# Optimization experiments

Measured on AMD Instinct MI355X. Metric: run time of the kernel, lower is better.

## Reference

```python
import jax, jax.numpy as jnp
import numpy as np

N_HEADS = 8
HEAD_DIM = 64  # d_model // n_heads = 512 // 8


def setup_inputs() -> dict:
    key = jax.random.key(0)
    kq, kk, kv, km = jax.random.split(key, 4)
    B, C, H, L, D = 8, 4, N_HEADS, 512, HEAD_DIM
    q = jax.random.normal(kq, (B * C, H, L, D), dtype=jnp.float32)
    k = jax.random.normal(kk, (B * C, H, D, L), dtype=jnp.float32)  # pre-transposed, matmul(q, k) directly
    v = jax.random.normal(kv, (B * C, H, L, D), dtype=jnp.float32)
    attn_mask = jax.random.randint(km, (B, L, L), 0, 2).astype(bool)  # True = masked out
    return {"q": q, "k": k, "v": v, "attn_mask": attn_mask}


def reference(q, k, v, attn_mask):
    # q: [B*C, H, L, D]; k: [B*C, H, D, L]; v: [B*C, H, L, D]; attn_mask: [B, L, L] bool
    scale = jnp.asarray(HEAD_DIM ** (-0.5), dtype=q.dtype)
    scores = jnp.einsum('ghld,ghdm->ghlm', q, k) * scale  # [B*C, H, L, L]
    if attn_mask is not None:
        B = attn_mask.shape[0]
        C = q.shape[0] // B
        H, L = scores.shape[1], scores.shape[2]
        scores = scores.reshape(B, C, H, L, L)
        mask = attn_mask[:, None, None, :, :]  # broadcast over channels and heads
        scores = jnp.where(mask, -jnp.inf, scores)
        scores = scores.reshape(B * C, H, L, L)
    attn_weights = jax.nn.softmax(scores, axis=-1)  # dropout p=0.0 -> identity (eval)
    output = jnp.einsum('ghlm,ghmd->ghld', attn_weights, v)  # [B*C, H, L, D]
    return output
```

## Files before the change

### kernel.cpp

```cpp
#include <hip/hip_runtime.h>


typedef __attribute__((ext_vector_type(8)))  short bf16x8;
typedef __attribute__((ext_vector_type(16))) float f32x16;

union Frag4 { uint4 x; unsigned u[4]; bf16x8 v; };

__device__ __forceinline__ unsigned pk_bf16(float a, float b){
    unsigned ua = __builtin_bit_cast(unsigned, a) + 0x8000u;
    unsigned ub = __builtin_bit_cast(unsigned, b) + 0x8000u;
    return __builtin_amdgcn_perm(ub, ua, 0x07060302u);
}

__device__ __forceinline__ float fast_exp2(float x){
#if __has_builtin(__builtin_amdgcn_exp2f)
    return __builtin_amdgcn_exp2f(x);
#else
    return exp2f(x);
#endif
}

#define L2E 1.44269504088896f

__global__ __launch_bounds__(256)
void pack_mask(const int* __restrict__ mg, unsigned long long* __restrict__ bits)
{
    const int t    = blockIdx.x*256 + threadIdx.x;
    const int lane = t & 63;
    const int w0   = t >> 6;
    const int strd = (int)((gridDim.x*256) >> 6);
    const int nW   = 8*512*8;
    for (int i = w0; i < nW; i += strd){
        int v = mg[(size_t)i*64 + lane];
        unsigned long long m = __ballot(v != 0);
        if (lane == 0) bits[i] = m;
    }
}

__device__ __forceinline__ unsigned build_mword(const int* p, int h){
    unsigned w = 0;
    #pragma unroll
    for (int rg=0; rg<4; ++rg){
        int4 mm = *(const int4*)(p + rg*8 + h*4);
        const unsigned base = rg*8 + h*4;
        w |= (mm.x?1u:0u) << base;
        w |= (mm.y?1u:0u) << (base+1);
        w |= (mm.z?1u:0u) << (base+2);
        w |= (mm.w?1u:0u) << (base+3);
    }
    return w;
}

template<int BITS>
__global__ __launch_bounds__(128, 4)
void attn_fused(const float* __restrict__ qg, const float* __restrict__ kg,
                const float* __restrict__ vg, const int* __restrict__ mg,
                const unsigned* __restrict__ bits, float* __restrict__ og)
{
    __shared__ uint4 sKt4[64*8];
    __shared__ uint4 sVt4[64*8];

    const int t    = threadIdx.x;
    const int lane = t & 63;
    const int wv   = t >> 6;
    const int col  = lane & 31;
    const int h    = lane >> 5;

    const int bi   = blockIdx.x;
    const int s    = bi >> 3;
    const int head = (bi & 7)*32 + (s >> 3);
    const int qt   = s & 7;
    const int b    = bi & 7;

    const float* qh = qg + (size_t)head*32768;
    const float* kh = kg + (size_t)head*32768;
    const float* vh = vg + (size_t)head*32768;
    float*       oh = og + (size_t)head*32768;

    const int qrl  = wv*32 + col;
    const int qrow = qt*64 + qrl;
    const int* mrow0 = BITS ? nullptr
        : mg + (size_t)b*262144 + (size_t)qrow*512;
    const unsigned* brow = BITS
        ? bits + ((size_t)b*512 + qrow)*16
        : nullptr;

    Frag4 qf[4];
    {
        const float* qr = qh + (size_t)qrow*64 + h*8;
        #pragma unroll
        for (int kt=0; kt<4; ++kt){
            float4 x0 = *(const float4*)(qr + kt*16);
            float4 x1 = *(const float4*)(qr + kt*16 + 4);
            qf[kt].u[0] = pk_bf16(x0.x*0.125f, x0.y*0.125f);
            qf[kt].u[1] = pk_bf16(x0.z*0.125f, x0.w*0.125f);
            qf[kt].u[2] = pk_bf16(x1.x*0.125f, x1.y*0.125f);
            qf[kt].u[3] = pk_bf16(x1.z*0.125f, x1.w*0.125f);
        }
    }

    f32x16 o0, o1;
    #pragma unroll
    for (int i=0;i<16;++i){ o0[i]=0.f; o1[i]=0.f; }
    float lsum = 0.f;

    for (int kb=0; kb<8; ++kb){
        __syncthreads();

        uint2 mbv;
        if constexpr (BITS) mbv = *(const uint2*)(brow + kb*2);

        #pragma unroll
        for (int gi=0; gi<4; ++gi){
            const int g = wv*4 + gi;
            const float* kp = kh + (size_t)(g*8)*512 + kb*64 + lane;
            float kv[8];
            #pragma unroll
            for (int dd=0; dd<8; ++dd) kv[dd] = kp[(size_t)dd*512];
            Frag4 w;
            w.u[0]=pk_bf16(kv[0],kv[1]); w.u[1]=pk_bf16(kv[2],kv[3]);
            w.u[2]=pk_bf16(kv[4],kv[5]); w.u[3]=pk_bf16(kv[6],kv[7]);
            sKt4[lane*8 + (g ^ (lane&7))] = w.x;
        }
        #pragma unroll
        for (int gi=0; gi<4; ++gi){
            const int g = wv*4 + gi;
            const float* vp = vh + (size_t)(kb*64 + g*8)*64 + lane;
            float vv[8];
            #pragma unroll
            for (int mm=0; mm<8; ++mm) vv[mm] = vp[(size_t)mm*64];
            Frag4 w;
            w.u[0]=pk_bf16(vv[0],vv[1]); w.u[1]=pk_bf16(vv[2],vv[3]);
            w.u[2]=pk_bf16(vv[4],vv[5]); w.u[3]=pk_bf16(vv[6],vv[7]);
            sVt4[lane*8 + (g ^ (lane&7))] = w.x;
        }
        __syncthreads();

        const int* mrow = BITS ? nullptr : (mrow0 + kb*64);
        #pragma unroll
        for (int mt=0; mt<2; ++mt){
            f32x16 sc;
            #pragma unroll
            for (int i=0;i<16;++i) sc[i]=0.f;
            #pragma unroll
            for (int kt=0; kt<4; ++kt){
                const int r = mt*32 + col;
                Frag4 a; a.x = sKt4[r*8 + ((kt*2+h) ^ (r&7))];
                sc = __builtin_amdgcn_mfma_f32_32x32x16_bf16(a.v, qf[kt].v, sc, 0, 0, 0);
            }
            unsigned pp[8];
            if constexpr (BITS){
                const unsigned mword = mt ? mbv.y : mbv.x;
                #pragma unroll
                for (int rg=0; rg<4; ++rg){
                    const unsigned mw = mword >> (rg*8 + h*4);
                    float e0 = (mw & 1u) ? 0.f : fast_exp2(sc[4*rg+0]*L2E);
                    float e1 = (mw & 2u) ? 0.f : fast_exp2(sc[4*rg+1]*L2E);
                    float e2 = (mw & 4u) ? 0.f : fast_exp2(sc[4*rg+2]*L2E);
                    float e3 = (mw & 8u) ? 0.f : fast_exp2(sc[4*rg+3]*L2E);
                    lsum += (e0+e1)+(e2+e3);
                    pp[2*rg]   = pk_bf16(e0, e1);
                    pp[2*rg+1] = pk_bf16(e2, e3);
                }
            } else {
                #pragma unroll
                for (int rg=0; rg<4; ++rg){
                    int4 mm = *(const int4*)(mrow + mt*32 + rg*8 + h*4);
                    float e0 = mm.x ? 0.f : fast_exp2(sc[4*rg+0]*L2E);
                    float e1 = mm.y ? 0.f : fast_exp2(sc[4*rg+1]*L2E);
                    float e2 = mm.z ? 0.f : fast_exp2(sc[4*rg+2]*L2E);
                    float e3 = mm.w ? 0.f : fast_exp2(sc[4*rg+3]*L2E);
                    lsum += (e0+e1)+(e2+e3);
                    pp[2*rg]   = pk_bf16(e0, e1);
                    pp[2*rg+1] = pk_bf16(e2, e3);
                }
            }

            #pragma unroll
            for (int c=0; c<2; ++c){
                unsigned keep0 = h ? pp[4*c+2] : pp[4*c+0];
                unsigned keep1 = h ? pp[4*c+3] : pp[4*c+1];
                unsigned give0 = h ? pp[4*c+0] : pp[4*c+2];
                unsigned give1 = h ? pp[4*c+1] : pp[4*c+3];
                unsigned got0 = (unsigned)__shfl_xor((int)give0, 32, 64);
                unsigned got1 = (unsigned)__shfl_xor((int)give1, 32, 64);
                Frag4 pa;
                pa.u[0] = h ? got0  : keep0;
                pa.u[1] = h ? got1  : keep1;
                pa.u[2] = h ? keep0 : got0;
                pa.u[3] = h ? keep1 : got1;
                const int gm = mt*4 + c*2 + h;
                Frag4 b0; b0.x = sVt4[col*8      + (gm ^ (col&7))];
                o0 = __builtin_amdgcn_mfma_f32_32x32x16_bf16(pa.v, b0.v, o0, 0, 0, 0);
                Frag4 b1; b1.x = sVt4[(32+col)*8 + (gm ^ ((32+col)&7))];
                o1 = __builtin_amdgcn_mfma_f32_32x32x16_bf16(pa.v, b1.v, o1, 0, 0, 0);
            }
        }
    }

    lsum += __shfl_xor(lsum, 32, 64);
    const float inv = 1.0f / lsum;
    float* ob = oh + (size_t)(qt*64 + wv*32)*64;
    #pragma unroll
    for (int r=0; r<16; ++r){
        const int qq = (r&3) + 8*(r>>2) + 4*h;
        const float iv = __shfl(inv, qq, 64);
        ob[(size_t)qq*64 + col]      = o0[r]*iv;
        ob[(size_t)qq*64 + 32 + col] = o1[r]*iv;
    }
}

extern "C" void kernel_launch(void* const* d_in, const int* in_sizes, int n_in,
                              void* d_out, int out_size, void* d_ws, size_t ws_size,
                              hipStream_t stream) {
    (void)in_sizes; (void)n_in; (void)out_size;
    const float* q = (const float*)d_in[0];
    const float* k = (const float*)d_in[1];
    const float* v = (const float*)d_in[2];
    const int*   m = (const int*)d_in[3];
    const size_t BITS_BYTES = (size_t)8*512*64;
    if (d_ws && ws_size >= BITS_BYTES){
        pack_mask<<<dim3(1024), dim3(256), 0, stream>>>(m, (unsigned long long*)d_ws);
        attn_fused<1><<<dim3(2048), dim3(128), 0, stream>>>(
            q, k, v, m, (const unsigned*)d_ws, (float*)d_out);
    } else {
        attn_fused<0><<<dim3(2048), dim3(128), 0, stream>>>(
            q, k, v, m, nullptr, (float*)d_out);
    }
}
```

Measured before the change: 194.4 us.

## Use 128-query blocks and split keys in halves with a combine kernel

Blocks grow to 256 threads covering 128 query rows, so each K/V tile staged in shared memory is reused by four waves instead of two. The key range is split into two halves handled by separate blocks, which write unnormalized partial outputs and row sums to workspace. A new combine kernel adds the halves and normalizes. This halves the redundant K/V conversion traffic per query row but adds partial-output writes and an extra kernel pass over the output.

```diff
diff --git a/kernel.cpp b/kernel.cpp
--- a/kernel.cpp
+++ b/kernel.cpp
@@ -51,11 +51,33 @@
     return w;
 }
 
-template<int BITS>
-__global__ __launch_bounds__(128, 4)
+__global__ __launch_bounds__(256)
+void combine_halves(const float4* __restrict__ oB,
+                    const float* __restrict__ lsums, float4* __restrict__ og)
+{
+    const size_t i0 = (size_t)blockIdx.x*256 + threadIdx.x;
+    #pragma unroll
+    for (int it=0; it<4; ++it){
+        const size_t idx = i0 + (size_t)it*524288;
+        const size_t row = idx >> 4;
+        const float la = lsums[row];
+        const float lb = lsums[row + 131072];
+        const float inv = 1.0f/(la+lb);
+        float4 a = og[idx], bq = oB[idx];
+        float4 r;
+        r.x=(a.x+bq.x)*inv; r.y=(a.y+bq.y)*inv;
+        r.z=(a.z+bq.z)*inv; r.w=(a.w+bq.w)*inv;
+        og[idx] = r;
+    }
+}
+
+template<int MODE>
+__global__ __launch_bounds__(256, 8)
 void attn_fused(const float* __restrict__ qg, const float* __restrict__ kg,
                 const float* __restrict__ vg, const int* __restrict__ mg,
-                const unsigned* __restrict__ bits, float* __restrict__ og)
+                const unsigned* __restrict__ bits,
+                float* __restrict__ oPart, float* __restrict__ lsums,
+                float* __restrict__ og)
 {
     __shared__ uint4 sKt4[64*8];
     __shared__ uint4 sVt4[64*8];
@@ -67,27 +89,26 @@
     const int h    = lane >> 5;
 
     const int bi   = blockIdx.x;
+    const int b    = bi & 7;
     const int s    = bi >> 3;
-    const int head = (bi & 7)*32 + (s >> 3);
-    const int qt   = s & 7;
-    const int b    = bi & 7;
+    int half, qt, head;
+    if constexpr (MODE==2){ half = s & 1; qt = (s>>1)&3; head = b*32 + (s>>3); }
+    else                  { half = 0;     qt = s & 3;    head = b*32 + (s>>2); }
 
     const float* qh = qg + (size_t)head*32768;
     const float* kh = kg + (size_t)head*32768;
     const float* vh = vg + (size_t)head*32768;
     float*       oh = og + (size_t)head*32768;
 
-    const int qrl  = wv*32 + col;
-    const int qrow = qt*64 + qrl;
-    const int* mrow0 = BITS ? nullptr
-        : mg + (size_t)b*262144 + (size_t)qrow*512;
-    const unsigned* brow = BITS
-        ? bits + ((size_t)b*512 + qrow)*16
-        : nullptr;
+    const int qrl = wv*32 + col;
+    const int* mrow0 = (MODE==0)
+        ? mg + (size_t)b*262144 + (size_t)(qt*128 + qrl)*512 : nullptr;
+    const unsigned* brow = (MODE>=1)
+        ? bits + ((size_t)b*512 + qt*128 + qrl)*16 : nullptr;
 
     Frag4 qf[4];
     {
-        const float* qr = qh + (size_t)qrow*64 + h*8;
+        const float* qr = qh + (size_t)(qt*128 + qrl)*64 + h*8;
         #pragma unroll
         for (int kt=0; kt<4; ++kt){
             float4 x0 = *(const float4*)(qr + kt*16);
@@ -104,15 +125,19 @@
     for (int i=0;i<16;++i){ o0[i]=0.f; o1[i]=0.f; }
     float lsum = 0.f;
 
-    for (int kb=0; kb<8; ++kb){
+    constexpr int NKB = (MODE==2) ? 4 : 8;
+    const int kb0 = (MODE==2) ? half*4 : 0;
+
+    for (int kk=0; kk<NKB; ++kk){
+        const int kb = kb0 + kk;
         __syncthreads();
 
         uint2 mbv;
-        if constexpr (BITS) mbv = *(const uint2*)(brow + kb*2);
-
-        #pragma unroll
-        for (int gi=0; gi<4; ++gi){
-            const int g = wv*4 + gi;
+        if constexpr (MODE>=1) mbv = *(const uint2*)(brow + kb*2);
+
+        #pragma unroll
+        for (int gi=0; gi<2; ++gi){
+            const int g = wv + gi*4;
             const float* kp = kh + (size_t)(g*8)*512 + kb*64 + lane;
             float kv[8];
             #pragma unroll
@@ -123,8 +148,8 @@
             sKt4[lane*8 + (g ^ (lane&7))] = w.x;
         }
         #pragma unroll
-        for (int gi=0; gi<4; ++gi){
-            const int g = wv*4 + gi;
+        for (int gi=0; gi<2; ++gi){
+            const int g = wv + gi*4;
             const float* vp = vh + (size_t)(kb*64 + g*8)*64 + lane;
             float vv[8];
             #pragma unroll
@@ -136,7 +161,7 @@
         }
         __syncthreads();
 
-        const int* mrow = BITS ? nullptr : (mrow0 + kb*64);
+        const int* mrow = (MODE==0) ? (mrow0 + kb*64) : nullptr;
         #pragma unroll
         for (int mt=0; mt<2; ++mt){
             f32x16 sc;
@@ -149,7 +174,7 @@
                 sc = __builtin_amdgcn_mfma_f32_32x32x16_bf16(a.v, qf[kt].v, sc, 0, 0, 0);
             }
             unsigned pp[8];
-            if constexpr (BITS){
+            if constexpr (MODE>=1){
                 const unsigned mword = mt ? mbv.y : mbv.x;
                 #pragma unroll
                 for (int rg=0; rg<4; ++rg){
@@ -199,14 +224,27 @@
     }
 
     lsum += __shfl_xor(lsum, 32, 64);
-    const float inv = 1.0f / lsum;
-    float* ob = oh + (size_t)(qt*64 + wv*32)*64;
-    #pragma unroll
-    for (int r=0; r<16; ++r){
-        const int qq = (r&3) + 8*(r>>2) + 4*h;
-        const float iv = __shfl(inv, qq, 64);
-        ob[(size_t)qq*64 + col]      = o0[r]*iv;
-        ob[(size_t)qq*64 + 32 + col] = o1[r]*iv;
+    if constexpr (MODE==2){
+        float* dst = (half ? oPart : og)
+                   + (size_t)head*32768 + (size_t)(qt*128 + wv*32)*64;
+        #pragma unroll
+        for (int r=0; r<16; ++r){
+            const int qq = (r&3) + 8*(r>>2) + 4*h;
+            dst[(size_t)qq*64 + col]      = o0[r];
+            dst[(size_t)qq*64 + 32 + col] = o1[r];
+        }
+        if (h == 0)
+            lsums[(size_t)half*131072 + (size_t)head*512 + qt*128 + wv*32 + col] = lsum;
+    } else {
+        const float inv = 1.0f / lsum;
+        float* ob = oh + (size_t)(qt*128 + wv*32)*64;
+        #pragma unroll
+        for (int r=0; r<16; ++r){
+            const int qq = (r&3) + 8*(r>>2) + 4*h;
+            const float iv = __shfl(inv, qq, 64);
+            ob[(size_t)qq*64 + col]      = o0[r]*iv;
+            ob[(size_t)qq*64 + 32 + col] = o1[r]*iv;
+        }
     }
 }
 
@@ -219,12 +257,26 @@
     const float* v = (const float*)d_in[2];
     const int*   m = (const int*)d_in[3];
     const size_t BITS_BYTES = (size_t)8*512*64;
-    if (d_ws && ws_size >= BITS_BYTES){
+    const size_t PART_OFF   = BITS_BYTES;
+    const size_t PART_BYTES = (size_t)256*512*64*4;
+    const size_t LS_OFF     = PART_OFF + PART_BYTES;
+    const size_t LS_BYTES   = (size_t)2*256*512*4;
+    const size_t TOTAL      = LS_OFF + LS_BYTES;
+
+    if (d_ws && ws_size >= TOTAL){
+        float* oPart = (float*)((char*)d_ws + PART_OFF);
+        float* lsums = (float*)((char*)d_ws + LS_OFF);
         pack_mask<<<dim3(1024), dim3(256), 0, stream>>>(m, (unsigned long long*)d_ws);
-        attn_fused<1><<<dim3(2048), dim3(128), 0, stream>>>(
-            q, k, v, m, (const unsigned*)d_ws, (float*)d_out);
+        attn_fused<2><<<dim3(2048), dim3(256), 0, stream>>>(
+            q, k, v, m, (const unsigned*)d_ws, oPart, lsums, (float*)d_out);
+        combine_halves<<<dim3(2048), dim3(256), 0, stream>>>(
+            (const float4*)oPart, lsums, (float4*)d_out);
+    } else if (d_ws && ws_size >= BITS_BYTES){
+        pack_mask<<<dim3(1024), dim3(256), 0, stream>>>(m, (unsigned long long*)d_ws);
+        attn_fused<1><<<dim3(1024), dim3(256), 0, stream>>>(
+            q, k, v, m, (const unsigned*)d_ws, nullptr, nullptr, (float*)d_out);
     } else {
-        attn_fused<0><<<dim3(2048), dim3(128), 0, stream>>>(
-            q, k, v, m, nullptr, (float*)d_out);
-    }
-}
+        attn_fused<0><<<dim3(1024), dim3(256), 0, stream>>>(
+            q, k, v, m, nullptr, nullptr, nullptr, (float*)d_out);
+    }
+}
```

After: 409.1 us. 2.1x slower.
